# Kernel optimization log

Hardware: AMD Instinct MI355X
Metric: run time of the kernel (lower is better)

The kernel has to match this reference:

```python
import jax, jax.numpy as jnp
import numpy as np
from jax import lax

SIGMA = 1.0
TRUNCATE = 4.0  # skimage.filters.gaussian default


def _gauss_kernel(sigma, truncate=TRUNCATE):
    radius = int(truncate * sigma + 0.5)
    t = np.arange(-radius, radius + 1, dtype=np.float32)
    k = np.exp(-0.5 * (t / sigma) ** 2)
    k = k / k.sum()
    return jnp.asarray(k), radius


def setup_inputs() -> dict:
    key = jax.random.key(0)
    x = jax.random.uniform(key, (128, 1, 512, 512), dtype=jnp.float32)
    return {"x": x}


def _blur(x, sigma=SIGMA):
    # x: [B, 1, H, W] -> squeeze channel like the torch module, blur, return [B, H, W]
    k, r = _gauss_kernel(sigma)
    K = 2 * r + 1
    # 'nearest' boundary mode of skimage == edge padding
    xp = jnp.pad(x, ((0, 0), (0, 0), (r, r), (r, r)), mode="edge")
    kh = k.reshape(1, 1, K, 1).astype(x.dtype)  # vertical pass
    kw = k.reshape(1, 1, 1, K).astype(x.dtype)  # horizontal pass
    dn = lax.conv_dimension_numbers(xp.shape, kh.shape, ("NCHW", "OIHW", "NCHW"))
    y = lax.conv_general_dilated(xp, kh, (1, 1), "VALID", dimension_numbers=dn)
    y = lax.conv_general_dilated(y, kw, (1, 1), "VALID", dimension_numbers=dn)
    return y[:, 0]  # [B, H, W], matching x_i.squeeze() per-sample output


def reference(x):
    return _blur(x)
```

## Files before the change

### kernel.cpp

```cpp
#include <hip/hip_runtime.h>
#include <stdint.h>

namespace {

constexpr int R     = 4;
constexpr int TSX   = 64;
constexpr int TSY   = 32;
constexpr int RAWH  = TSY + 2 * R;
constexpr int RF4   = 19;
constexpr int RSTRF = RF4 * 4;
constexpr int NRAW4 = RAWH * RF4;
constexpr int NCHUNK = 12;
constexpr int HSTR  = 68;
constexpr int IMG_H = 512;
constexpr int IMG_W = 512;
constexpr int NHP   = RAWH * (TSX / 4);

__device__ __forceinline__ int clampi(int v, int lo, int hi) {
    return v < lo ? lo : (v > hi ? hi : v);
}

__global__ __launch_bounds__(256)
void gauss_blur_kernel(const float* __restrict__ in, float* __restrict__ out) {
    const float KW[9] = {
        1.3383062e-4f, 4.4318616e-3f, 5.3990966e-2f, 2.4197144e-1f,
        3.9894347e-1f, 2.4197144e-1f, 5.3990966e-2f, 4.4318616e-3f,
        1.3383062e-4f};

    __shared__ float s_raw[NCHUNK * 256];
    __shared__ float s_h  [RAWH * HSTR];

    const int tid  = threadIdx.x;
    const int lane = tid & 63;
    const int wave = tid >> 6;
    const int b    = blockIdx.z;
    const int ty0  = blockIdx.y * TSY;
    const int tx0  = blockIdx.x * TSX;

    const float* __restrict__ inb = in + (size_t)b * IMG_H * IMG_W;

    const bool x_interior = (blockIdx.x >= 1) && (blockIdx.x + 1 < IMG_W / TSX);

    if (x_interior) {
        #pragma unroll
        for (int k = 0; k < 3; ++k) {
            const int q  = wave * 3 + k;
            const int f  = (q << 6) | lane;
            const int ru = (int)((unsigned)f / 19u);
            const int c  = f - 19 * ru;
            const int r  = ru > RAWH - 1 ? RAWH - 1 : ru;
            const int gy = clampi(ty0 - R + r, 0, IMG_H - 1);
            const float* src = inb + (size_t)gy * IMG_W + (tx0 - R + 4 * c);
            __builtin_amdgcn_global_load_lds(
                (const __attribute__((address_space(1))) uint32_t*)src,
                (__attribute__((address_space(3))) uint32_t*)(s_raw + (q << 8)),
                16, 0, 0);
        }
    } else {
        for (int i = tid; i < NRAW4; i += 256) {
            const int r  = (int)((unsigned)i / 19u);
            const int c  = i - 19 * r;
            const int gy = clampi(ty0 - R + r, 0, IMG_H - 1);
            const float* rp = inb + (size_t)gy * IMG_W;
            const int gx = tx0 - R + 4 * c;
            float4 v;
            v.x = rp[clampi(gx + 0, 0, IMG_W - 1)];
            v.y = rp[clampi(gx + 1, 0, IMG_W - 1)];
            v.z = rp[clampi(gx + 2, 0, IMG_W - 1)];
            v.w = rp[clampi(gx + 3, 0, IMG_W - 1)];
            *reinterpret_cast<float4*>(&s_raw[(r * RF4 + c) * 4]) = v;
        }
    }
    __syncthreads();

    for (int i = tid; i < NHP; i += 256) {
        const int r = i >> 4, j = i & 15;
        const float* rp = &s_raw[r * RSTRF + 4 * j];
        float4 a  = *reinterpret_cast<const float4*>(rp);
        float4 bq = *reinterpret_cast<const float4*>(rp + 4);
        float4 cq = *reinterpret_cast<const float4*>(rp + 8);
        float w[12] = {a.x, a.y, a.z, a.w, bq.x, bq.y, bq.z, bq.w,
                       cq.x, cq.y, cq.z, cq.w};
        float a0 = 0.f, a1 = 0.f, a2 = 0.f, a3 = 0.f;
        #pragma unroll
        for (int t = 0; t < 9; ++t) {
            a0 = fmaf(KW[t], w[t + 0], a0);
            a1 = fmaf(KW[t], w[t + 1], a1);
            a2 = fmaf(KW[t], w[t + 2], a2);
            a3 = fmaf(KW[t], w[t + 3], a3);
        }
        float4 o = {a0, a1, a2, a3};
        *reinterpret_cast<float4*>(&s_h[r * HSTR + 4 * j]) = o;
    }
    __syncthreads();

    const int px  = tid & 15;
    const int py  = tid >> 4;
    const int lx  = 4 * px;
    const int oy0 = 2 * py;

    float4 acc0 = {0.f, 0.f, 0.f, 0.f};
    float4 acc1 = {0.f, 0.f, 0.f, 0.f};
    #pragma unroll
    for (int t = 0; t < 10; ++t) {
        float4 h = *reinterpret_cast<const float4*>(&s_h[(oy0 + t) * HSTR + lx]);
        if (t < 9) {
            acc0.x = fmaf(KW[t], h.x, acc0.x);
            acc0.y = fmaf(KW[t], h.y, acc0.y);
            acc0.z = fmaf(KW[t], h.z, acc0.z);
            acc0.w = fmaf(KW[t], h.w, acc0.w);
        }
        if (t >= 1) {
            acc1.x = fmaf(KW[t - 1], h.x, acc1.x);
            acc1.y = fmaf(KW[t - 1], h.y, acc1.y);
            acc1.z = fmaf(KW[t - 1], h.z, acc1.z);
            acc1.w = fmaf(KW[t - 1], h.w, acc1.w);
        }
    }

    float* __restrict__ outb = out + (size_t)b * IMG_H * IMG_W;
    *reinterpret_cast<float4*>(&outb[(size_t)(ty0 + oy0) * IMG_W + tx0 + lx]) = acc0;
    *reinterpret_cast<float4*>(&outb[(size_t)(ty0 + oy0 + 1) * IMG_W + tx0 + lx]) = acc1;
}

}

extern "C" void kernel_launch(void* const* d_in, const int* in_sizes, int n_in,
                              void* d_out, int out_size, void* d_ws, size_t ws_size,
                              hipStream_t stream) {
    const float* x = (const float*)d_in[0];
    float* out = (float*)d_out;

    const int batch = in_sizes[0] / (IMG_H * IMG_W);

    dim3 grid(IMG_W / TSX, IMG_H / TSY, batch);
    gauss_blur_kernel<<<grid, 256, 0, stream>>>(x, out);
}
```

Baseline: 62.60 us.

## Make blocks persistent over image columns with double-buffered async LDS loads

```diff
diff --git a/kernel.cpp b/kernel.cpp
--- a/kernel.cpp
+++ b/kernel.cpp
@@ -3,18 +3,15 @@
 
 namespace {
 
-constexpr int R     = 4;
+constexpr int IMG   = 512;
 constexpr int TSX   = 64;
-constexpr int TSY   = 32;
-constexpr int RAWH  = TSY + 2 * R;
-constexpr int RF4   = 19;
-constexpr int RSTRF = RF4 * 4;
-constexpr int NRAW4 = RAWH * RF4;
-constexpr int NCHUNK = 12;
+constexpr int STEP  = 32;
+constexpr int RAWR  = STEP + 8;
+constexpr int RSTR  = 76;
+constexpr int NCH   = 12;
+constexpr int RBUF  = NCH * 256;
 constexpr int HSTR  = 68;
-constexpr int IMG_H = 512;
-constexpr int IMG_W = 512;
-constexpr int NHP   = RAWH * (TSX / 4);
+constexpr int NSTEP = IMG / STEP;
 
 __device__ __forceinline__ int clampi(int v, int lo, int hi) {
     return v < lo ? lo : (v > hi ? hi : v);
@@ -27,100 +24,124 @@
         3.9894347e-1f, 2.4197144e-1f, 5.3990966e-2f, 4.4318616e-3f,
         1.3383062e-4f};
 
-    __shared__ float s_raw[NCHUNK * 256];
-    __shared__ float s_h  [RAWH * HSTR];
+    __shared__ float s_raw[2][RBUF];
+    __shared__ float s_h[RAWR * HSTR];
 
     const int tid  = threadIdx.x;
     const int lane = tid & 63;
     const int wave = tid >> 6;
-    const int b    = blockIdx.z;
-    const int ty0  = blockIdx.y * TSY;
-    const int tx0  = blockIdx.x * TSX;
+    const int bx   = blockIdx.x;
+    const int b    = blockIdx.y;
+    const int tx0  = bx * TSX;
+    const bool isL = (bx == 0);
+    const bool isR = (bx == (IMG / TSX) - 1);
 
-    const float* __restrict__ inb = in + (size_t)b * IMG_H * IMG_W;
+    const float* __restrict__ inb  = in  + (size_t)b * IMG * IMG;
+    float* __restrict__       outb = out + (size_t)b * IMG * IMG;
 
-    const bool x_interior = (blockIdx.x >= 1) && (blockIdx.x + 1 < IMG_W / TSX);
-
-    if (x_interior) {
+    auto issue = [&](int tk, int buf) {
         #pragma unroll
-        for (int k = 0; k < 3; ++k) {
-            const int q  = wave * 3 + k;
+        for (int c = 0; c < 3; ++c) {
+            const int q  = wave * 3 + c;
             const int f  = (q << 6) | lane;
-            const int ru = (int)((unsigned)f / 19u);
-            const int c  = f - 19 * ru;
-            const int r  = ru > RAWH - 1 ? RAWH - 1 : ru;
-            const int gy = clampi(ty0 - R + r, 0, IMG_H - 1);
-            const float* src = inb + (size_t)gy * IMG_W + (tx0 - R + 4 * c);
+            unsigned ru  = (unsigned)f / 19u;
+            const int cf = f - 19 * (int)ru;
+            int r = (int)ru; if (r > RAWR - 1) r = RAWR - 1;
+            const int gy = clampi(STEP * tk - 4 + r, 0, IMG - 1);
+            int gx = tx0 - 4 + 4 * cf;
+            gx = clampi(gx, 0, IMG - 4);
+            const float* src = inb + (size_t)gy * IMG + gx;
             __builtin_amdgcn_global_load_lds(
                 (const __attribute__((address_space(1))) uint32_t*)src,
-                (__attribute__((address_space(3))) uint32_t*)(s_raw + (q << 8)),
+                (__attribute__((address_space(3))) uint32_t*)(&s_raw[buf][0] + (q << 8)),
                 16, 0, 0);
         }
-    } else {
-        for (int i = tid; i < NRAW4; i += 256) {
-            const int r  = (int)((unsigned)i / 19u);
-            const int c  = i - 19 * r;
-            const int gy = clampi(ty0 - R + r, 0, IMG_H - 1);
-            const float* rp = inb + (size_t)gy * IMG_W;
-            const int gx = tx0 - R + 4 * c;
-            float4 v;
-            v.x = rp[clampi(gx + 0, 0, IMG_W - 1)];
-            v.y = rp[clampi(gx + 1, 0, IMG_W - 1)];
-            v.z = rp[clampi(gx + 2, 0, IMG_W - 1)];
-            v.w = rp[clampi(gx + 3, 0, IMG_W - 1)];
-            *reinterpret_cast<float4*>(&s_raw[(r * RF4 + c) * 4]) = v;
+    };
+
+    issue(0, 0);
+
+    #pragma unroll 1
+    for (int k = 0; k < NSTEP; ++k) {
+        const int buf = k & 1;
+
+        if (k + 1 < NSTEP) {
+            issue(k + 1, buf ^ 1);
+            asm volatile("s_waitcnt vmcnt(3)" ::: "memory");
+        } else {
+            asm volatile("s_waitcnt vmcnt(0)" ::: "memory");
         }
+        __builtin_amdgcn_sched_barrier(0);
+        __builtin_amdgcn_s_barrier();
+
+        if (isL | isR) {
+            for (int t = tid; t < RAWR; t += 256) {
+                float* row = &s_raw[buf][t * RSTR];
+                if (isL) {
+                    const float e = row[4];
+                    float4 s = {e, e, e, e};
+                    *reinterpret_cast<float4*>(&row[0]) = s;
+                } else {
+                    const float e = row[67];
+                    float4 s = {e, e, e, e};
+                    *reinterpret_cast<float4*>(&row[68]) = s;
+                    *reinterpret_cast<float4*>(&row[72]) = s;
+                }
+            }
+        }
+        asm volatile("s_waitcnt lgkmcnt(0)" ::: "memory");
+        __builtin_amdgcn_sched_barrier(0);
+        __builtin_amdgcn_s_barrier();
+
+        for (int i = tid; i < RAWR * 16; i += 256) {
+            const int r = i >> 4, j = i & 15;
+            const float* rp = &s_raw[buf][r * RSTR + 4 * j];
+            float4 a  = *reinterpret_cast<const float4*>(rp);
+            float4 bq = *reinterpret_cast<const float4*>(rp + 4);
+            float4 cq = *reinterpret_cast<const float4*>(rp + 8);
+            const float w[12] = {a.x, a.y, a.z, a.w, bq.x, bq.y, bq.z, bq.w,
+                                 cq.x, cq.y, cq.z, cq.w};
+            float a0 = 0.f, a1 = 0.f, a2 = 0.f, a3 = 0.f;
+            #pragma unroll
+            for (int t = 0; t < 9; ++t) {
+                a0 = fmaf(KW[t], w[t + 0], a0);
+                a1 = fmaf(KW[t], w[t + 1], a1);
+                a2 = fmaf(KW[t], w[t + 2], a2);
+                a3 = fmaf(KW[t], w[t + 3], a3);
+            }
+            float4 o = {a0, a1, a2, a3};
+            *reinterpret_cast<float4*>(&s_h[r * HSTR + 4 * j]) = o;
+        }
+        asm volatile("s_waitcnt lgkmcnt(0)" ::: "memory");
+        __builtin_amdgcn_sched_barrier(0);
+        __builtin_amdgcn_s_barrier();
+
+        const int px  = tid & 15;
+        const int py  = tid >> 4;
+        const int lx  = 4 * px;
+        const int oy0 = 2 * py;
+
+        float4 acc0 = {0.f, 0.f, 0.f, 0.f};
+        float4 acc1 = {0.f, 0.f, 0.f, 0.f};
+        #pragma unroll
+        for (int t = 0; t < 10; ++t) {
+            float4 h = *reinterpret_cast<const float4*>(&s_h[(oy0 + t) * HSTR + lx]);
+            if (t < 9) {
+                acc0.x = fmaf(KW[t], h.x, acc0.x);
+                acc0.y = fmaf(KW[t], h.y, acc0.y);
+                acc0.z = fmaf(KW[t], h.z, acc0.z);
+                acc0.w = fmaf(KW[t], h.w, acc0.w);
+            }
+            if (t >= 1) {
+                acc1.x = fmaf(KW[t - 1], h.x, acc1.x);
+                acc1.y = fmaf(KW[t - 1], h.y, acc1.y);
+                acc1.z = fmaf(KW[t - 1], h.z, acc1.z);
+                acc1.w = fmaf(KW[t - 1], h.w, acc1.w);
+            }
+        }
+        const int y = STEP * k + oy0;
+        *reinterpret_cast<float4*>(&outb[(size_t)y * IMG + tx0 + lx])       = acc0;
+        *reinterpret_cast<float4*>(&outb[(size_t)(y + 1) * IMG + tx0 + lx]) = acc1;
     }
-    __syncthreads();
-
-    for (int i = tid; i < NHP; i += 256) {
-        const int r = i >> 4, j = i & 15;
-        const float* rp = &s_raw[r * RSTRF + 4 * j];
-        float4 a  = *reinterpret_cast<const float4*>(rp);
-        float4 bq = *reinterpret_cast<const float4*>(rp + 4);
-        float4 cq = *reinterpret_cast<const float4*>(rp + 8);
-        float w[12] = {a.x, a.y, a.z, a.w, bq.x, bq.y, bq.z, bq.w,
-                       cq.x, cq.y, cq.z, cq.w};
-        float a0 = 0.f, a1 = 0.f, a2 = 0.f, a3 = 0.f;
-        #pragma unroll
-        for (int t = 0; t < 9; ++t) {
-            a0 = fmaf(KW[t], w[t + 0], a0);
-            a1 = fmaf(KW[t], w[t + 1], a1);
-            a2 = fmaf(KW[t], w[t + 2], a2);
-            a3 = fmaf(KW[t], w[t + 3], a3);
-        }
-        float4 o = {a0, a1, a2, a3};
-        *reinterpret_cast<float4*>(&s_h[r * HSTR + 4 * j]) = o;
-    }
-    __syncthreads();
-
-    const int px  = tid & 15;
-    const int py  = tid >> 4;
-    const int lx  = 4 * px;
-    const int oy0 = 2 * py;
-
-    float4 acc0 = {0.f, 0.f, 0.f, 0.f};
-    float4 acc1 = {0.f, 0.f, 0.f, 0.f};
-    #pragma unroll
-    for (int t = 0; t < 10; ++t) {
-        float4 h = *reinterpret_cast<const float4*>(&s_h[(oy0 + t) * HSTR + lx]);
-        if (t < 9) {
-            acc0.x = fmaf(KW[t], h.x, acc0.x);
-            acc0.y = fmaf(KW[t], h.y, acc0.y);
-            acc0.z = fmaf(KW[t], h.z, acc0.z);
-            acc0.w = fmaf(KW[t], h.w, acc0.w);
-        }
-        if (t >= 1) {
-            acc1.x = fmaf(KW[t - 1], h.x, acc1.x);
-            acc1.y = fmaf(KW[t - 1], h.y, acc1.y);
-            acc1.z = fmaf(KW[t - 1], h.z, acc1.z);
-            acc1.w = fmaf(KW[t - 1], h.w, acc1.w);
-        }
-    }
-
-    float* __restrict__ outb = out + (size_t)b * IMG_H * IMG_W;
-    *reinterpret_cast<float4*>(&outb[(size_t)(ty0 + oy0) * IMG_W + tx0 + lx]) = acc0;
-    *reinterpret_cast<float4*>(&outb[(size_t)(ty0 + oy0 + 1) * IMG_W + tx0 + lx]) = acc1;
 }
 
 }
@@ -131,8 +152,8 @@
     const float* x = (const float*)d_in[0];
     float* out = (float*)d_out;
 
-    const int batch = in_sizes[0] / (IMG_H * IMG_W);
+    const int batch = in_sizes[0] / (IMG * IMG);
 
-    dim3 grid(IMG_W / TSX, IMG_H / TSY, batch);
+    dim3 grid(IMG / TSX, batch);
     gauss_blur_kernel<<<grid, 256, 0, stream>>>(x, out);
 }
```

New measurement: 69.37 us. 10.8% more time.
